# Kernel optimization log

Measured on AMD Instinct MI355X. Metric: run time of the kernel, lower is better.

Reference implementation:

```python
import jax, jax.numpy as jnp
import numpy as np

B, S, D, H = 4, 2048, 1024, 16
DK = D // H


def setup_inputs() -> dict:
    key = jax.random.key(0)
    ks = jax.random.split(key, 10)
    s = 0.02  # keep linear outputs well-scaled
    causal = jnp.triu(jnp.ones((S, S), dtype=bool), k=1)  # True = masked
    return {
        "Q": jax.random.normal(ks[0], (B, S, D), dtype=jnp.float32),
        "K_V": jax.random.normal(ks[1], (B, S, D), dtype=jnp.float32),
        "mask": jnp.broadcast_to(causal, (B, S, S)),
        "Wq": jax.random.normal(ks[2], (D, D), dtype=jnp.float32) * s,
        "bq": jnp.zeros((D,), dtype=jnp.float32),
        "Wk": jax.random.normal(ks[3], (D, D), dtype=jnp.float32) * s,
        "bk": jnp.zeros((D,), dtype=jnp.float32),
        "Wv": jax.random.normal(ks[4], (D, D), dtype=jnp.float32) * s,
        "bv": jnp.zeros((D,), dtype=jnp.float32),
        "Wo": jax.random.normal(ks[5], (D, D), dtype=jnp.float32) * s,
        "bo": jnp.zeros((D,), dtype=jnp.float32),
    }


def reference(Q, K_V, mask, Wq, bq, Wk, bk, Wv, bv, Wo, bo):
    # Linear projections
    q = Q @ Wq + bq          # [B, Sq, D]
    k = K_V @ Wk + bk        # [B, Sk, D]
    v = K_V @ Wv + bv        # [B, Sk, D]
    Sq, Sk = q.shape[1], k.shape[1]
    # chunk(dim=2)+cat(dim=0) == split into H heads of size DK
    q = q.reshape(B, Sq, H, DK)
    k = k.reshape(B, Sk, H, DK)
    v = v.reshape(B, Sk, H, DK)
    scale = 1.0 / jnp.sqrt(jnp.float32(DK))
    scores = jnp.einsum("bqhd,bkhd->bhqk", q, k) * scale  # [B,H,Sq,Sk]
    # mask.repeat(head_num,1,1) == broadcast mask over heads
    scores = jnp.where(mask[:, None, :, :], -jnp.inf, scores)
    attn = jax.nn.softmax(scores, axis=-1)
    # dropout is identity in eval mode
    out = jnp.einsum("bhqk,bkhd->bqhd", attn, v).reshape(B, Sq, D)
    return out @ Wo + bo
```

## Files before the change

### kernel.cpp

```cpp
#include <hip/hip_runtime.h>

typedef unsigned short u16;
typedef __attribute__((ext_vector_type(8))) __bf16 bf16x8;
typedef __attribute__((ext_vector_type(4))) float f32x4;

#define B_  4
#define S_  2048
#define D_  1024
#define H_  16
#define DK_ 64

__device__ __forceinline__ u16 f2bf(float f) {
  unsigned u = __float_as_uint(f);
  u += 0x7fffu + ((u >> 16) & 1u);
  return (u16)(u >> 16);
}
__device__ __forceinline__ float hexp2(float f) {
  return __builtin_amdgcn_exp2f(f);
}
__device__ __forceinline__ unsigned pack_bf2(float f0, float f1) {
  return __builtin_amdgcn_perm(__float_as_uint(f1), __float_as_uint(f0), 0x07060302u);
}

__device__ __forceinline__ void load_lds16(const u16* g, u16* l) {
  __builtin_amdgcn_global_load_lds((const __attribute__((address_space(1))) void*)g,
                                   (__attribute__((address_space(3))) void*)l,
                                   16, 0, 0);
}

__global__ void cvt_bf16_2(const float* __restrict__ x0, u16* __restrict__ y0,
                           const float* __restrict__ x1, u16* __restrict__ y1, int n4) {
  int i = blockIdx.x * blockDim.x + threadIdx.x;
  const float* x = x0; u16* y = y0;
  int j = i;
  if (i >= n4) { x = x1; y = y1; j = i - n4; }
  float4 v = ((const float4*)x)[j];
  ushort4 o;
  o.x = f2bf(v.x); o.y = f2bf(v.y); o.z = f2bf(v.z); o.w = f2bf(v.w);
  ((ushort4*)y)[j] = o;
}

__global__ void transpose_cvt4(const float* __restrict__ W0, const float* __restrict__ W1,
                               const float* __restrict__ W2, const float* __restrict__ W3,
                               u16* __restrict__ T0, u16* __restrict__ T1,
                               u16* __restrict__ T2, u16* __restrict__ T3) {
  __shared__ float tile[32][33];
  const float* W = (blockIdx.z == 0) ? W0 : (blockIdx.z == 1) ? W1 : (blockIdx.z == 2) ? W2 : W3;
  u16*         T = (blockIdx.z == 0) ? T0 : (blockIdx.z == 1) ? T1 : (blockIdx.z == 2) ? T2 : T3;
  int bx = blockIdx.x * 32, by = blockIdx.y * 32;
  int tx = threadIdx.x, ty = threadIdx.y;
  #pragma unroll
  for (int i = 0; i < 32; i += 8)
    tile[ty + i][tx] = W[(size_t)(by + ty + i) * D_ + bx + tx];
  __syncthreads();
  #pragma unroll
  for (int i = 0; i < 32; i += 8)
    T[(size_t)(bx + ty + i) * D_ + by + tx] = f2bf(tile[tx][ty + i]);
}

#define GBM 128
#define GBN 256
#define GNT 16

template<int MODE>
__global__ __launch_bounds__(512, 2)
void gemm8p(const u16* __restrict__ Aq, const u16* __restrict__ Ak,
            const u16* __restrict__ Bt,
            const float* __restrict__ bq, const float* __restrict__ bk,
            const float* __restrict__ bv,
            u16* __restrict__ qp, u16* __restrict__ kp, u16* __restrict__ vpT,
            float* __restrict__ Cf, float qscale) {
  __shared__ __align__(16) u16 sm[2 * 24576];
  const int tid  = threadIdx.x;
  const int lane = tid & 63, wave = tid >> 6;
  const int bm = blockIdx.x * GBM;
  const int bn = blockIdx.y * GBN;
  const int wm = (wave >> 2) * 64, wn = (wave & 3) * 64;
  const int fm = lane & 15, fk4 = lane >> 4;
  const int K = D_;

  int path = 0;
  const u16* A = Aq;
  if constexpr (MODE == 0) { path = bn >> 10; if (path != 0) A = Ak; }

  const int sr  = tid >> 2;
  const int sl  = tid & 3;
  const int kof = (sl ^ (sr & 3)) * 8;
  const u16* gA  = A  + (size_t)(bm + sr) * K + kof;
  const u16* gB0 = Bt + (size_t)(bn + sr) * K + kof;
  const u16* gB1 = Bt + (size_t)(bn + 128 + sr) * K + kof;

#define GR(t, ks) do { \
    u16* lr_ = &sm[((t) & 1) * 24576 + (ks) * 12288]; \
    const int ko_ = (t) * 64 + (ks) * 32; \
    load_lds16(gA  + ko_, lr_ + tid * 8); \
    load_lds16(gB0 + ko_, lr_ + 4096 + tid * 8); \
    load_lds16(gB1 + ko_, lr_ + 8192 + tid * 8); \
  } while (0)

  const int sfrag = (fk4 ^ (fm & 3)) * 8;
  f32x4 acc[4][4] = {};

  GR(0, 0);
  asm volatile("" ::: "memory");
  GR(0, 1);
  asm volatile("" ::: "memory");
  GR(1, 0);

  #pragma unroll
  for (int t = 0; t < GNT; ++t) {
    #pragma unroll
    for (int ks = 0; ks < 2; ++ks) {
      if (t < GNT - 1)  asm volatile("s_waitcnt vmcnt(6)" ::: "memory");
      else if (ks == 0) asm volatile("s_waitcnt vmcnt(3)" ::: "memory");
      else              asm volatile("s_waitcnt vmcnt(0)" ::: "memory");
      __builtin_amdgcn_s_barrier();
      if (ks == 0) { if (t + 1 < GNT) GR(t + 1, 1); }
      else         { if (t + 2 < GNT) GR(t + 2, 0); }
      asm volatile("" ::: "memory");

      const u16* rb = &sm[(t & 1) * 24576 + ks * 12288];
      bf16x8 af[4], bfr[4];
      #pragma unroll
      for (int m = 0; m < 4; ++m)
        af[m] = *(const bf16x8*)&rb[(wm + m * 16 + fm) * 32 + sfrag];
      #pragma unroll
      for (int j = 0; j < 4; ++j)
        bfr[j] = *(const bf16x8*)&rb[(128 + wn + j * 16 + fm) * 32 + sfrag];
      asm volatile("s_waitcnt lgkmcnt(0)" ::: "memory");
      __builtin_amdgcn_s_setprio(1);
      #pragma unroll
      for (int m = 0; m < 4; ++m)
        #pragma unroll
        for (int j = 0; j < 4; ++j)
          acc[m][j] = __builtin_amdgcn_mfma_f32_16x16x32_bf16(af[m], bfr[j], acc[m][j], 0, 0, 0);
      __builtin_amdgcn_s_setprio(0);
    }
  }
#undef GR

  if constexpr (MODE == 0) {
    #pragma unroll
    for (int i = 0; i < 4; ++i) {
      #pragma unroll
      for (int j = 0; j < 4; ++j) {
        int colg = bn + wn + j * 16 + fm;
        int rowg0 = bm + wm + i * 16 + fk4 * 4;
        if (path == 0) {
          float bb = bq[colg];
          #pragma unroll
          for (int rg = 0; rg < 4; ++rg)
            qp[(size_t)(rowg0 + rg) * D_ + colg] = f2bf((acc[i][j][rg] + bb) * qscale);
        } else if (path == 1) {
          int ck = colg - 1024;
          float bb = bk[ck];
          #pragma unroll
          for (int rg = 0; rg < 4; ++rg)
            kp[(size_t)(rowg0 + rg) * D_ + ck] = f2bf(acc[i][j][rg] + bb);
        } else {
          int cv = colg - 2048;
          float bb = bv[cv];
          int hh = cv >> 6, dk = cv & 63;
          int bbt = rowg0 >> 11, s = rowg0 & (S_ - 1);
          ushort4 pk4;
          pk4.x = f2bf(acc[i][j][0] + bb);
          pk4.y = f2bf(acc[i][j][1] + bb);
          pk4.z = f2bf(acc[i][j][2] + bb);
          pk4.w = f2bf(acc[i][j][3] + bb);
          *(ushort4*)&vpT[(((size_t)bbt * H_ + hh) * DK_ + dk) * S_ + s] = pk4;
        }
      }
    }
  } else {
    #pragma unroll
    for (int i = 0; i < 4; ++i)
      #pragma unroll
      for (int j = 0; j < 4; ++j) {
        int colg = bn + wn + j * 16 + fm;
        float bb = bq[colg];
        #pragma unroll
        for (int rg = 0; rg < 4; ++rg) {
          int rowg = bm + wm + i * 16 + fk4 * 4 + rg;
          Cf[(size_t)rowg * D_ + colg] = acc[i][j][rg] + bb;
        }
      }
  }
}

__global__ __launch_bounds__(256, 3)
void attn_kernel(const u16* __restrict__ qp, const u16* __restrict__ kp,
                 const u16* __restrict__ vpT, u16* __restrict__ ao) {
  __shared__ u16 Ks[16 * 512];
  __shared__ u16 Vs[16 * 512];
  __shared__ u16 Ps[4 * 4 * 512];

  const int tid  = threadIdx.x;
  const int lane = tid & 63;
  const int w    = tid >> 6;
  const int fm   = lane & 15;
  const int fk4  = lane >> 4;

  const int i  = blockIdx.x;
  const int qt = 15 - (i >> 6);
  const int bh = i & 63;
  const int b  = bh >> 4;
  const int h  = bh & 15;

  const int q0 = qt * 128 + w * 32;
  const int nj = qt + 1;

  u16* Pw = &Ps[w * 2048];
  const u16* kb = kp  + (size_t)(b * S_) * D_ + h * DK_;
  const u16* vb = vpT + (size_t)((b * H_ + h) * DK_) * S_;

  bf16x8 aq[2][2];
  #pragma unroll
  for (int qf = 0; qf < 2; ++qf)
    #pragma unroll
    for (int kh = 0; kh < 2; ++kh)
      aq[qf][kh] = *(const bf16x8*)(qp + (size_t)(b * S_ + q0 + qf * 16 + fm) * D_
                                       + h * DK_ + kh * 32 + fk4 * 8);

  f32x4 oacc[2][4] = {};
  float l0 = 0.f, l1 = 0.f;

  #pragma unroll 1
  for (int j = 0; j < nj; ++j) {
    const int kv0 = j * 128;
    const bool lastt = (j == qt);

    __syncthreads();
    #pragma unroll
    for (int c = 0; c < 4; ++c) {
      int idx = 4 * w + c;
      load_lds16(kb + (size_t)(kv0 + (idx >> 1) * 16 + fm) * D_ + (idx & 1) * 32 + fk4 * 8,
                 &Ks[idx * 512 + lane * 8]);
    }
    #pragma unroll
    for (int c = 0; c < 4; ++c) {
      int idx = 4 * w + c;
      load_lds16(vb + (size_t)((idx & 3) * 16 + fm) * S_ + kv0 + (idx >> 2) * 32 + fk4 * 8,
                 &Vs[idx * 512 + lane * 8]);
    }
    __syncthreads();

    #pragma unroll
    for (int h2 = 0; h2 < 2; ++h2) {
      #pragma unroll
      for (int mtl = 0; mtl < 4; ++mtl) {
        const int mt = h2 * 4 + mtl;
        bf16x8 kf0 = *(const bf16x8*)&Ks[(mt * 2 + 0) * 512 + lane * 8];
        bf16x8 kf1 = *(const bf16x8*)&Ks[(mt * 2 + 1) * 512 + lane * 8];
        f32x4 z0 = {0.f, 0.f, 0.f, 0.f}, z1 = z0;
        z0 = __builtin_amdgcn_mfma_f32_16x16x32_bf16(kf0, aq[0][0], z0, 0, 0, 0);
        z0 = __builtin_amdgcn_mfma_f32_16x16x32_bf16(kf1, aq[0][1], z0, 0, 0, 0);
        z1 = __builtin_amdgcn_mfma_f32_16x16x32_bf16(kf0, aq[1][0], z1, 0, 0, 0);
        z1 = __builtin_amdgcn_mfma_f32_16x16x32_bf16(kf1, aq[1][1], z1, 0, 0, 0);

        const int kvr = kv0 + mt * 16 + fk4 * 4;
        float e0[4], e1[4];
        #pragma unroll
        for (int rg = 0; rg < 4; ++rg) {
          float zz0 = z0[rg], zz1 = z1[rg];
          if (lastt) {
            if (kvr + rg > q0 + fm)      zz0 = -1e30f;
            if (kvr + rg > q0 + 16 + fm) zz1 = -1e30f;
          }
          e0[rg] = hexp2(zz0);
          e1[rg] = hexp2(zz1);
          l0 += e0[rg]; l1 += e1[rg];
        }
        const int ktl  = mtl >> 1;
        const int fk4c = (mt & 1) * 2 + (fk4 >> 1);
        const int woff = ((fk4c * 16 + fm) * 8 + (fk4 & 1) * 4);
        uint2 w0, w1;
        w0.x = pack_bf2(e0[0], e0[1]); w0.y = pack_bf2(e0[2], e0[3]);
        w1.x = pack_bf2(e1[0], e1[1]); w1.y = pack_bf2(e1[2], e1[3]);
        *(uint2*)&Pw[(ktl * 2 + 0) * 512 + woff] = w0;
        *(uint2*)&Pw[(ktl * 2 + 1) * 512 + woff] = w1;
      }

      #pragma unroll
      for (int ktl = 0; ktl < 2; ++ktl) {
        const int kt = h2 * 2 + ktl;
        bf16x8 ap0 = *(const bf16x8*)&Pw[(ktl * 2 + 0) * 512 + lane * 8];
        bf16x8 ap1 = *(const bf16x8*)&Pw[(ktl * 2 + 1) * 512 + lane * 8];
        #pragma unroll
        for (int nt = 0; nt < 4; ++nt) {
          bf16x8 bv = *(const bf16x8*)&Vs[(kt * 4 + nt) * 512 + lane * 8];
          oacc[0][nt] = __builtin_amdgcn_mfma_f32_16x16x32_bf16(ap0, bv, oacc[0][nt], 0, 0, 0);
          oacc[1][nt] = __builtin_amdgcn_mfma_f32_16x16x32_bf16(ap1, bv, oacc[1][nt], 0, 0, 0);
        }
      }
    }
  }

  #pragma unroll
  for (int qf = 0; qf < 2; ++qf) {
    float ls = (qf == 0) ? l0 : l1;
    ls += __shfl_xor(ls, 16, 64);
    ls += __shfl_xor(ls, 32, 64);
    #pragma unroll
    for (int rg = 0; rg < 4; ++rg) {
      float lr = __shfl(ls, fk4 * 4 + rg, 64);
      float inv = 1.0f / lr;
      int q = q0 + qf * 16 + fk4 * 4 + rg;
      #pragma unroll
      for (int nt = 0; nt < 4; ++nt) {
        float o = oacc[qf][nt][rg] * inv;
        ao[(size_t)(b * S_ + q) * D_ + h * DK_ + nt * 16 + fm] = f2bf(o);
      }
    }
  }
}

extern "C" void kernel_launch(void* const* d_in, const int* in_sizes, int n_in,
                              void* d_out, int out_size, void* d_ws, size_t ws_size,
                              hipStream_t stream) {
  const float* Q  = (const float*)d_in[0];
  const float* KV = (const float*)d_in[1];
  const float* Wq = (const float*)d_in[3];
  const float* bq = (const float*)d_in[4];
  const float* Wk = (const float*)d_in[5];
  const float* bk = (const float*)d_in[6];
  const float* Wv = (const float*)d_in[7];
  const float* bv = (const float*)d_in[8];
  const float* Wo = (const float*)d_in[9];
  const float* bo = (const float*)d_in[10];
  float* out = (float*)d_out;

  char* ws = (char*)d_ws;
  u16* Qb  = (u16*)(ws);
  u16* Kb  = (u16*)(ws + (16ull << 20));
  u16* Wqt = (u16*)(ws + (32ull << 20));
  u16* Wkt = (u16*)(ws + (34ull << 20));
  u16* Wvt = (u16*)(ws + (36ull << 20));
  u16* Wot = (u16*)(ws + (38ull << 20));
  u16* qp  = (u16*)(ws + (40ull << 20));
  u16* kp  = (u16*)(ws + (56ull << 20));
  u16* vpT = (u16*)(ws + (72ull << 20));
  u16* ao  = Qb;

  const int n4 = (B_ * S_ * D_) / 4;
  cvt_bf16_2<<<2 * n4 / 256, 256, 0, stream>>>(Q, Qb, KV, Kb, n4);

  transpose_cvt4<<<dim3(32, 32, 4), dim3(32, 8), 0, stream>>>(Wq, Wk, Wv, Wo,
                                                              Wqt, Wkt, Wvt, Wot);

  const float qscale = 0.125f * 1.44269504f;
  gemm8p<0><<<dim3(8192 / GBM, 3072 / GBN), 512, 0, stream>>>(
      Qb, Kb, Wqt, bq, bk, bv, qp, kp, vpT, nullptr, qscale);

  attn_kernel<<<1024, 256, 0, stream>>>(qp, kp, vpT, ao);

  gemm8p<1><<<dim3(8192 / GBM, 1024 / GBN), 512, 0, stream>>>(
      ao, nullptr, Wot, bo, nullptr, nullptr, nullptr, nullptr, nullptr, out, 1.0f);
}
```

Before: 332.3 us.

## Triple-buffer GEMM with BK=64 tiles and double-buffer K/V in attention

The GEMM now uses a three-stage LDS ring of 64-wide K slabs with an 8-way XOR swizzle and one barrier per K step instead of two. The attention kernel double-buffers K/V tiles so the next tile's global loads overlap current compute, swizzles the P scratch writes and reads to avoid LDS bank conflicts, and raises MFMA priority with setprio. Both changes grow LDS use: the GEMM buffer goes from 96 KB to 144 KB per block, and attention occupancy drops from 3 to 2 blocks per CU.

```diff
diff --git a/kernel.cpp b/kernel.cpp
--- a/kernel.cpp
+++ b/kernel.cpp
@@ -70,7 +70,7 @@
             const float* __restrict__ bv,
             u16* __restrict__ qp, u16* __restrict__ kp, u16* __restrict__ vpT,
             float* __restrict__ Cf, float qscale) {
-  __shared__ __align__(16) u16 sm[2 * 24576];
+  __shared__ __align__(16) u16 sm[3 * 24576];
   const int tid  = threadIdx.x;
   const int lane = tid & 63, wave = tid >> 6;
   const int bm = blockIdx.x * GBM;
@@ -83,22 +83,24 @@
   const u16* A = Aq;
   if constexpr (MODE == 0) { path = bn >> 10; if (path != 0) A = Ak; }
 
-  const int sr  = tid >> 2;
-  const int sl  = tid & 3;
-  const int kof = (sl ^ (sr & 3)) * 8;
-  const u16* gA  = A  + (size_t)(bm + sr) * K + kof;
-  const u16* gB0 = Bt + (size_t)(bn + sr) * K + kof;
-  const u16* gB1 = Bt + (size_t)(bn + 128 + sr) * K + kof;
-
-#define GR(t, ks) do { \
-    u16* lr_ = &sm[((t) & 1) * 24576 + (ks) * 12288]; \
-    const int ko_ = (t) * 64 + (ks) * 32; \
-    load_lds16(gA  + ko_, lr_ + tid * 8); \
-    load_lds16(gB0 + ko_, lr_ + 4096 + tid * 8); \
-    load_lds16(gB1 + ko_, lr_ + 8192 + tid * 8); \
-  } while (0)
-
-  const int sfrag = (fk4 ^ (fm & 3)) * 8;
+  const int sr0 = tid >> 3;
+  const int kof = ((tid & 7) ^ (sr0 & 7)) * 8;
+  const u16* gA = A  + (size_t)(bm + sr0) * K + kof;
+  const u16* gB = Bt + (size_t)(bn + sr0) * K + kof;
+
+#define GR(t, g) do { \
+    u16* d_ = &sm[((t) % 3) * 24576 + (g) * 12288]; \
+    const int ko_ = (t) * 64; \
+    if ((g) == 0) { \
+      load_lds16(gA + ko_,           d_ + tid * 8); \
+      load_lds16(gA + 64 * K + ko_,  d_ + 4096 + tid * 8); \
+      load_lds16(gB + ko_,           d_ + 8192 + tid * 8); \
+    } else { \
+      load_lds16(gB + 64 * K + ko_,  d_ + tid * 8); \
+      load_lds16(gB + 128 * K + ko_, d_ + 4096 + tid * 8); \
+      load_lds16(gB + 192 * K + ko_, d_ + 8192 + tid * 8); \
+    } } while (0)
+
   f32x4 acc[4][4] = {};
 
   GR(0, 0);
@@ -106,27 +108,29 @@
   GR(0, 1);
   asm volatile("" ::: "memory");
   GR(1, 0);
+  asm volatile("" ::: "memory");
+  GR(1, 1);
 
   #pragma unroll
   for (int t = 0; t < GNT; ++t) {
+    if (t < GNT - 1) asm volatile("s_waitcnt vmcnt(6)" ::: "memory");
+    else             asm volatile("s_waitcnt vmcnt(0)" ::: "memory");
+    __builtin_amdgcn_s_barrier();
+
     #pragma unroll
     for (int ks = 0; ks < 2; ++ks) {
-      if (t < GNT - 1)  asm volatile("s_waitcnt vmcnt(6)" ::: "memory");
-      else if (ks == 0) asm volatile("s_waitcnt vmcnt(3)" ::: "memory");
-      else              asm volatile("s_waitcnt vmcnt(0)" ::: "memory");
-      __builtin_amdgcn_s_barrier();
-      if (ks == 0) { if (t + 1 < GNT) GR(t + 1, 1); }
-      else         { if (t + 2 < GNT) GR(t + 2, 0); }
+      if (t + 2 < GNT) GR(t + 2, ks);
       asm volatile("" ::: "memory");
 
-      const u16* rb = &sm[(t & 1) * 24576 + ks * 12288];
+      const u16* rb = &sm[(t % 3) * 24576];
+      const int slot = (((ks * 4) + fk4) ^ (fm & 7)) * 8;
       bf16x8 af[4], bfr[4];
       #pragma unroll
       for (int m = 0; m < 4; ++m)
-        af[m] = *(const bf16x8*)&rb[(wm + m * 16 + fm) * 32 + sfrag];
+        af[m] = *(const bf16x8*)&rb[(wm + m * 16 + fm) * 64 + slot];
       #pragma unroll
       for (int j = 0; j < 4; ++j)
-        bfr[j] = *(const bf16x8*)&rb[(128 + wn + j * 16 + fm) * 32 + sfrag];
+        bfr[j] = *(const bf16x8*)&rb[(128 + wn + j * 16 + fm) * 64 + slot];
       asm volatile("s_waitcnt lgkmcnt(0)" ::: "memory");
       __builtin_amdgcn_s_setprio(1);
       #pragma unroll
@@ -187,11 +191,11 @@
   }
 }
 
-__global__ __launch_bounds__(256, 3)
+__global__ __launch_bounds__(256, 2)
 void attn_kernel(const u16* __restrict__ qp, const u16* __restrict__ kp,
                  const u16* __restrict__ vpT, u16* __restrict__ ao) {
-  __shared__ u16 Ks[16 * 512];
-  __shared__ u16 Vs[16 * 512];
+  __shared__ u16 Ks[2][16 * 512];
+  __shared__ u16 Vs[2][16 * 512];
   __shared__ u16 Ps[4 * 4 * 512];
 
   const int tid  = threadIdx.x;
@@ -199,6 +203,7 @@
   const int w    = tid >> 6;
   const int fm   = lane & 15;
   const int fk4  = lane >> 4;
+  const int csl  = (lane ^ ((lane >> 3) & 7)) * 8;
 
   const int i  = blockIdx.x;
   const int qt = 15 - (i >> 6);
@@ -213,6 +218,21 @@
   const u16* kb = kp  + (size_t)(b * S_) * D_ + h * DK_;
   const u16* vb = vpT + (size_t)((b * H_ + h) * DK_) * S_;
 
+#define STAGEKV(bf, jj) do { \
+    const int kv0_ = (jj) * 128; \
+    _Pragma("unroll") \
+    for (int c = 0; c < 4; ++c) { \
+      int idx = 4 * w + c; \
+      load_lds16(kb + (size_t)(kv0_ + (idx >> 1) * 16 + fm) * D_ + (idx & 1) * 32 + fk4 * 8, \
+                 &Ks[bf][idx * 512 + lane * 8]); \
+    } \
+    _Pragma("unroll") \
+    for (int c = 0; c < 4; ++c) { \
+      int idx = 4 * w + c; \
+      load_lds16(vb + (size_t)((idx & 3) * 16 + fm) * S_ + kv0_ + (idx >> 2) * 32 + fk4 * 8, \
+                 &Vs[bf][idx * 512 + lane * 8]); \
+    } } while (0)
+
   bf16x8 aq[2][2];
   #pragma unroll
   for (int qf = 0; qf < 2; ++qf)
@@ -223,39 +243,40 @@
 
   f32x4 oacc[2][4] = {};
   float l0 = 0.f, l1 = 0.f;
+
+  STAGEKV(0, 0);
 
   #pragma unroll 1
   for (int j = 0; j < nj; ++j) {
     const int kv0 = j * 128;
     const bool lastt = (j == qt);
 
-    __syncthreads();
-    #pragma unroll
-    for (int c = 0; c < 4; ++c) {
-      int idx = 4 * w + c;
-      load_lds16(kb + (size_t)(kv0 + (idx >> 1) * 16 + fm) * D_ + (idx & 1) * 32 + fk4 * 8,
-                 &Ks[idx * 512 + lane * 8]);
-    }
-    #pragma unroll
-    for (int c = 0; c < 4; ++c) {
-      int idx = 4 * w + c;
-      load_lds16(vb + (size_t)((idx & 3) * 16 + fm) * S_ + kv0 + (idx >> 2) * 32 + fk4 * 8,
-                 &Vs[idx * 512 + lane * 8]);
-    }
-    __syncthreads();
+    __builtin_amdgcn_s_barrier();
+    if (j + 1 < nj) {
+      STAGEKV((j + 1) & 1, j + 1);
+      asm volatile("s_waitcnt vmcnt(8)" ::: "memory");
+    } else {
+      asm volatile("s_waitcnt vmcnt(0)" ::: "memory");
+    }
+    __builtin_amdgcn_s_barrier();
+
+    const u16* Kb_ = &Ks[j & 1][0];
+    const u16* Vb_ = &Vs[j & 1][0];
 
     #pragma unroll
     for (int h2 = 0; h2 < 2; ++h2) {
       #pragma unroll
       for (int mtl = 0; mtl < 4; ++mtl) {
         const int mt = h2 * 4 + mtl;
-        bf16x8 kf0 = *(const bf16x8*)&Ks[(mt * 2 + 0) * 512 + lane * 8];
-        bf16x8 kf1 = *(const bf16x8*)&Ks[(mt * 2 + 1) * 512 + lane * 8];
+        bf16x8 kf0 = *(const bf16x8*)&Kb_[(mt * 2 + 0) * 512 + lane * 8];
+        bf16x8 kf1 = *(const bf16x8*)&Kb_[(mt * 2 + 1) * 512 + lane * 8];
         f32x4 z0 = {0.f, 0.f, 0.f, 0.f}, z1 = z0;
+        __builtin_amdgcn_s_setprio(1);
         z0 = __builtin_amdgcn_mfma_f32_16x16x32_bf16(kf0, aq[0][0], z0, 0, 0, 0);
         z0 = __builtin_amdgcn_mfma_f32_16x16x32_bf16(kf1, aq[0][1], z0, 0, 0, 0);
         z1 = __builtin_amdgcn_mfma_f32_16x16x32_bf16(kf0, aq[1][0], z1, 0, 0, 0);
         z1 = __builtin_amdgcn_mfma_f32_16x16x32_bf16(kf1, aq[1][1], z1, 0, 0, 0);
+        __builtin_amdgcn_s_setprio(0);
 
         const int kvr = kv0 + mt * 16 + fk4 * 4;
         float e0[4], e1[4];
@@ -272,7 +293,8 @@
         }
         const int ktl  = mtl >> 1;
         const int fk4c = (mt & 1) * 2 + (fk4 >> 1);
-        const int woff = ((fk4c * 16 + fm) * 8 + (fk4 & 1) * 4);
+        const int c    = fk4c * 16 + fm;
+        const int woff = (c ^ ((c >> 3) & 7)) * 8 + (fk4 & 1) * 4;
         uint2 w0, w1;
         w0.x = pack_bf2(e0[0], e0[1]); w0.y = pack_bf2(e0[2], e0[3]);
         w1.x = pack_bf2(e1[0], e1[1]); w1.y = pack_bf2(e1[2], e1[3]);
@@ -283,17 +305,20 @@
       #pragma unroll
       for (int ktl = 0; ktl < 2; ++ktl) {
         const int kt = h2 * 2 + ktl;
-        bf16x8 ap0 = *(const bf16x8*)&Pw[(ktl * 2 + 0) * 512 + lane * 8];
-        bf16x8 ap1 = *(const bf16x8*)&Pw[(ktl * 2 + 1) * 512 + lane * 8];
+        bf16x8 ap0 = *(const bf16x8*)&Pw[(ktl * 2 + 0) * 512 + csl];
+        bf16x8 ap1 = *(const bf16x8*)&Pw[(ktl * 2 + 1) * 512 + csl];
+        __builtin_amdgcn_s_setprio(1);
         #pragma unroll
         for (int nt = 0; nt < 4; ++nt) {
-          bf16x8 bv = *(const bf16x8*)&Vs[(kt * 4 + nt) * 512 + lane * 8];
+          bf16x8 bv = *(const bf16x8*)&Vb_[(kt * 4 + nt) * 512 + lane * 8];
           oacc[0][nt] = __builtin_amdgcn_mfma_f32_16x16x32_bf16(ap0, bv, oacc[0][nt], 0, 0, 0);
           oacc[1][nt] = __builtin_amdgcn_mfma_f32_16x16x32_bf16(ap1, bv, oacc[1][nt], 0, 0, 0);
         }
+        __builtin_amdgcn_s_setprio(0);
       }
     }
   }
+#undef STAGEKV
 
   #pragma unroll
   for (int qf = 0; qf < 2; ++qf) {
```

After: 322.2 us. 3.0% less time.
